# Kernel optimization log

Measured on AMD Instinct MI355X. Metric: run time of the kernel, lower is better.

Reference implementation:

```python
import jax, jax.numpy as jnp
import numpy as np

ALPHA = 20.0  # SuperSpike surrogate sharpness
V_TH = 1.0
DT = 1.0

@jax.custom_vjp
def heaviside(x):
    return (x > 0).astype(x.dtype)

def _heaviside_fwd(x):
    return heaviside(x), x

def _heaviside_bwd(x, g):
    # SuperSpike surrogate gradient: 1 / (alpha*|x| + 1)^2
    return (g / (ALPHA * jnp.abs(x) + 1.0) ** 2,)

heaviside.defvjp(_heaviside_fwd, _heaviside_bwd)


def setup_inputs() -> dict:
    key = jax.random.key(0)
    k1, k2 = jax.random.split(key)
    B, T, IN, H = 128, 2000, 16, 256
    x = jax.random.normal(k1, (B, T, IN), dtype=jnp.float32)
    W = jax.random.normal(k2, (H, IN), dtype=jnp.float32) / np.sqrt(IN)
    tau_syn = jnp.full((1, H), 0.1, dtype=jnp.float32)
    tau_mem = jnp.full((1, H), 0.05, dtype=jnp.float32)
    return {"x": x, "W": W, "tau_syn": tau_syn, "tau_mem": tau_mem}


def reference(x, W, tau_syn, tau_mem):
    """SNNEncode forward: linear input projection + LIF recurrence over time.
    x: [B,T,IN], W: [H,IN], taus: [1,H]. Returns (spikes [T,B,H], (v,i) final state)."""
    tau_syn_inv = jnp.clip(tau_syn, 0.0, 1.0)  # [1,H]
    tau_mem_inv = jnp.clip(tau_mem, 0.0, 1.0)  # [1,H]

    B, T, IN = x.shape
    H = W.shape[0]
    # project all timesteps at once: [T,B,H]
    xw = jnp.einsum("bti,hi->tbh", x, W)

    def step(state, inp_t):
        v, i = state
        # norse lif_feed_forward_step (v_leak = 0, v_reset = 0)
        v_dec = v + DT * tau_mem_inv * (-v + i)
        i_dec = i + DT * (-tau_syn_inv) * i
        z = heaviside(v_dec - V_TH)
        v_new = (1.0 - z) * v_dec
        i_new = i_dec + inp_t
        return (v_new, i_new), z

    zeros = jnp.zeros((B, H), dtype=x.dtype)
    (v_f, i_f), spikes = jax.lax.scan(step, (zeros, zeros), xw)
    return spikes, v_f, i_f
```

## Files before the change

kernel.cpp:

```cpp
#include <hip/hip_runtime.h>


constexpr int B  = 128;
constexpr int T  = 2000;
constexpr int IN = 16;
constexpr int H  = 256;
constexpr int BH = B * H;
constexpr int CH = 256;

typedef float f4 __attribute__((ext_vector_type(4)));

__global__ __launch_bounds__(128, 1) void snn_named(
    const float* __restrict__ x, const float* __restrict__ Wm,
    const float* __restrict__ tau_syn, const float* __restrict__ tau_mem,
    float* __restrict__ out)
{
#pragma clang fp contract(off)
  const int tid = threadIdx.x, bid = blockIdx.x;
  const int b = bid >> 1;
  const int h = ((bid & 1) << 7) | tid;

  float w[IN];
#pragma unroll
  for (int k = 0; k < IN; ++k) w[k] = Wm[h * IN + k];

  float ts = tau_syn[h]; ts = ts < 0.f ? 0.f : (ts > 1.f ? 1.f : ts);
  float tm = tau_mem[h]; tm = tm < 0.f ? 0.f : (tm > 1.f ? 1.f : tm);
  const float nts = -ts;

  const char* xbc = (const char*)(x + (size_t)b * T * IN);
  const f4*   xb4 = (const f4*)xbc;
  float* op = out + (size_t)b * H + h;
  float vS = 0.f, iS = 0.f;

  auto TOUCH = [&](int r0) {
    const int lim = T * 4 - 1;
#pragma unroll
    for (int i = 0; i < 8; ++i) {
      int idx = r0 * 4 + tid + i * 128;
      idx = idx > lim ? lim : idx;
      f4 d = xb4[idx];
      asm volatile("" :: "v"(d.x), "v"(d.y), "v"(d.z), "v"(d.w));
    }
  };

  f4 A0, A1, A2, A3, A4, A5, A6, A7;
  f4 Bg0, Bg1, Bg2, Bg3, Bg4, Bg5, Bg6, Bg7;
  f4 C0, C1, C2, C3, C4, C5, C6, C7;
  f4 D0, D1, D2, D3, D4, D5, D6, D7;

#define LOADG(P0_, P1_, P2_, P3_, P4_, P5_, P6_, P7_, r)                 \
  do {                                                                   \
    int ra_ = (r);                                                       \
    ra_ = ra_ > (T - 2) ? (T - 2) : ra_;                                 \
    int off_ = ra_ * (IN * 4);                                           \
    asm("" : "+v"(off_));                  \
    const f4* q_ = (const f4*)(xbc + off_);                              \
    P0_ = q_[0]; P1_ = q_[1]; P2_ = q_[2]; P3_ = q_[3];                  \
    P4_ = q_[4]; P5_ = q_[5]; P6_ = q_[6]; P7_ = q_[7];                  \
  } while (0)

#define LIF1(xwv)                                                        \
  do {                                                                   \
    const float t1_ = iS - vS;                                           \
    const float t2_ = tm * t1_;                                          \
    const float vd_ = vS + t2_;                                          \
    const float xm_ = vd_ - 1.0f;                                        \
    const bool  sp_ = xm_ > 0.0f;                                        \
    vS = sp_ ? 0.0f : vd_;                                               \
    const float t3_ = nts * iS;                                          \
    const float id_ = iS + t3_;                                          \
    iS = id_ + (xwv);                                                    \
    __builtin_nontemporal_store(sp_ ? 1.0f : 0.0f, op);                  \
    op += BH;                                                            \
  } while (0)

#define DOT4(Q0_, Q1_, Q2_, Q3_, dst_)                                   \
  do {                                                                   \
    float a_ = 0.0f;                                                     \
    a_ = __builtin_fmaf(Q0_[0], w[0],  a_);                              \
    a_ = __builtin_fmaf(Q0_[1], w[1],  a_);                              \
    a_ = __builtin_fmaf(Q0_[2], w[2],  a_);                              \
    a_ = __builtin_fmaf(Q0_[3], w[3],  a_);                              \
    a_ = __builtin_fmaf(Q1_[0], w[4],  a_);                              \
    a_ = __builtin_fmaf(Q1_[1], w[5],  a_);                              \
    a_ = __builtin_fmaf(Q1_[2], w[6],  a_);                              \
    a_ = __builtin_fmaf(Q1_[3], w[7],  a_);                              \
    a_ = __builtin_fmaf(Q2_[0], w[8],  a_);                              \
    a_ = __builtin_fmaf(Q2_[1], w[9],  a_);                              \
    a_ = __builtin_fmaf(Q2_[2], w[10], a_);                              \
    a_ = __builtin_fmaf(Q2_[3], w[11], a_);                              \
    a_ = __builtin_fmaf(Q3_[0], w[12], a_);                              \
    a_ = __builtin_fmaf(Q3_[1], w[13], a_);                              \
    a_ = __builtin_fmaf(Q3_[2], w[14], a_);                              \
    a_ = __builtin_fmaf(Q3_[3], w[15], a_);                              \
    dst_ = a_;                                                           \
  } while (0)

#define STEP2G(P0_, P1_, P2_, P3_, P4_, P5_, P6_, P7_)                   \
  do {                                                                   \
    float xwa_, xwb_;                                                    \
    DOT4(P0_, P1_, P2_, P3_, xwa_);                                      \
    DOT4(P4_, P5_, P6_, P7_, xwb_);                                      \
    LIF1(xwa_);                                                          \
    LIF1(xwb_);                                                          \
  } while (0)

  TOUCH(0);
  TOUCH(CH);
  LOADG(A0, A1, A2, A3, A4, A5, A6, A7, 0);
  LOADG(Bg0, Bg1, Bg2, Bg3, Bg4, Bg5, Bg6, Bg7, 2);
  LOADG(C0, C1, C2, C3, C4, C5, C6, C7, 4);
  LOADG(D0, D1, D2, D3, D4, D5, D6, D7, 6);

  for (int t0 = 0; t0 < T; t0 += 8) {
    if ((t0 & (CH - 1)) == 0) TOUCH(t0 + 2 * CH);
    STEP2G(A0, A1, A2, A3, A4, A5, A6, A7);
    LOADG(A0, A1, A2, A3, A4, A5, A6, A7, t0 + 8);
    STEP2G(Bg0, Bg1, Bg2, Bg3, Bg4, Bg5, Bg6, Bg7);
    LOADG(Bg0, Bg1, Bg2, Bg3, Bg4, Bg5, Bg6, Bg7, t0 + 10);
    STEP2G(C0, C1, C2, C3, C4, C5, C6, C7);
    LOADG(C0, C1, C2, C3, C4, C5, C6, C7, t0 + 12);
    STEP2G(D0, D1, D2, D3, D4, D5, D6, D7);
    LOADG(D0, D1, D2, D3, D4, D5, D6, D7, t0 + 14);
  }

  out[(size_t)T * BH + (size_t)b * H + h]      = vS;
  out[(size_t)T * BH + BH + (size_t)b * H + h] = iS;
}

extern "C" void kernel_launch(void* const* d_in, const int* in_sizes, int n_in,
                              void* d_out, int out_size, void* d_ws, size_t ws_size,
                              hipStream_t stream) {
  const float* x  = (const float*)d_in[0];
  const float* W  = (const float*)d_in[1];
  const float* ts = (const float*)d_in[2];
  const float* tm = (const float*)d_in[3];
  float* out = (float*)d_out;
  hipLaunchKernelGGL(snn_named, dim3(B * 2), dim3(128), 0, stream,
                     x, W, ts, tm, out);
}
```

Baseline: 447.4 us.

## Buffer spike bits in a register and store them one tile late

Spike flags are no longer stored on every step. Each one is packed into a 32-bit register, and the previous tile's 32 spikes are written out interleaved with the next tile's compute, which takes store issue off the serial recurrence. The L2 prefetch is also reworked from an 8-load touch every 256 steps to a single-load touch per 32-step tile. In exchange the code gains tail handling for the last 16 steps and more complex index math, with some risk of off-by-one errors in the delayed stores.

```diff
diff --git a/kernel.cpp b/kernel.cpp
--- a/kernel.cpp
+++ b/kernel.cpp
@@ -6,11 +6,13 @@
 constexpr int IN = 16;
 constexpr int H  = 256;
 constexpr int BH = B * H;
-constexpr int CH = 256;
+constexpr int TILE = 32;
+constexpr int NTILE = 62;
+constexpr int TAIL = 16;
 
 typedef float f4 __attribute__((ext_vector_type(4)));
 
-__global__ __launch_bounds__(128, 1) void snn_named(
+__global__ __launch_bounds__(128, 1) void snn_bl(
     const float* __restrict__ x, const float* __restrict__ Wm,
     const float* __restrict__ tau_syn, const float* __restrict__ tau_mem,
     float* __restrict__ out)
@@ -30,10 +32,11 @@
 
   const char* xbc = (const char*)(x + (size_t)b * T * IN);
   const f4*   xb4 = (const f4*)xbc;
-  float* op = out + (size_t)b * H + h;
+  float* ob = out + (size_t)b * H + h;
   float vS = 0.f, iS = 0.f;
-
-  auto TOUCH = [&](int r0) {
+  unsigned bits = 0u, bitsPrev = 0u;
+
+  auto TOUCH8 = [&](int r0) {
     const int lim = T * 4 - 1;
 #pragma unroll
     for (int i = 0; i < 8; ++i) {
@@ -43,6 +46,13 @@
       asm volatile("" :: "v"(d.x), "v"(d.y), "v"(d.z), "v"(d.w));
     }
   };
+  auto TOUCH1 = [&](int r0) {
+    const int lim = T * 4 - 1;
+    int idx = r0 * 4 + tid;
+    idx = idx > lim ? lim : idx;
+    f4 d = xb4[idx];
+    asm volatile("" :: "v"(d.x), "v"(d.y), "v"(d.z), "v"(d.w));
+  };
 
   f4 A0, A1, A2, A3, A4, A5, A6, A7;
   f4 Bg0, Bg1, Bg2, Bg3, Bg4, Bg5, Bg6, Bg7;
@@ -54,7 +64,7 @@
     int ra_ = (r);                                                       \
     ra_ = ra_ > (T - 2) ? (T - 2) : ra_;                                 \
     int off_ = ra_ * (IN * 4);                                           \
-    asm("" : "+v"(off_));                  \
+    asm("" : "+v"(off_));                 \
     const f4* q_ = (const f4*)(xbc + off_);                              \
     P0_ = q_[0]; P1_ = q_[1]; P2_ = q_[2]; P3_ = q_[3];                  \
     P4_ = q_[4]; P5_ = q_[5]; P6_ = q_[6]; P7_ = q_[7];                  \
@@ -71,8 +81,7 @@
     const float t3_ = nts * iS;                                          \
     const float id_ = iS + t3_;                                          \
     iS = id_ + (xwv);                                                    \
-    __builtin_nontemporal_store(sp_ ? 1.0f : 0.0f, op);                  \
-    op += BH;                                                            \
+    bits = (bits >> 1) | (sp_ ? 0x80000000u : 0u);                       \
   } while (0)
 
 #define DOT4(Q0_, Q1_, Q2_, Q3_, dst_)                                   \
@@ -106,15 +115,56 @@
     LIF1(xwb_);                                                          \
   } while (0)
 
-  TOUCH(0);
-  TOUCH(CH);
+#define STORE8(t0_, r_)                                                  \
+  do {                                                                   \
+    _Pragma("unroll")                                                    \
+    for (int j_ = 0; j_ < 8; ++j_) {                                     \
+      int rr_ = (t0_) - TILE + 8 * (r_) + j_;                            \
+      rr_ = rr_ < 0 ? 0 : rr_;                                           \
+      const float fv_ =                                                  \
+          ((bitsPrev >> (8 * (r_) + j_)) & 1u) ? 1.0f : 0.0f;            \
+      __builtin_nontemporal_store(fv_, ob + ((size_t)rr_ << 15));        \
+    }                                                                    \
+  } while (0)
+
+  TOUCH8(0);
+  TOUCH8(256);
   LOADG(A0, A1, A2, A3, A4, A5, A6, A7, 0);
   LOADG(Bg0, Bg1, Bg2, Bg3, Bg4, Bg5, Bg6, Bg7, 2);
   LOADG(C0, C1, C2, C3, C4, C5, C6, C7, 4);
   LOADG(D0, D1, D2, D3, D4, D5, D6, D7, 6);
 
-  for (int t0 = 0; t0 < T; t0 += 8) {
-    if ((t0 & (CH - 1)) == 0) TOUCH(t0 + 2 * CH);
+#define ROT(t0_, r_)                                                     \
+  do {                                                                   \
+    STORE8(t0_, r_);                                                     \
+    STEP2G(A0, A1, A2, A3, A4, A5, A6, A7);                              \
+    LOADG(A0, A1, A2, A3, A4, A5, A6, A7, (t0_) + 8 * (r_) + 8);         \
+    STEP2G(Bg0, Bg1, Bg2, Bg3, Bg4, Bg5, Bg6, Bg7);                      \
+    LOADG(Bg0, Bg1, Bg2, Bg3, Bg4, Bg5, Bg6, Bg7, (t0_) + 8 * (r_) + 10);\
+    STEP2G(C0, C1, C2, C3, C4, C5, C6, C7);                              \
+    LOADG(C0, C1, C2, C3, C4, C5, C6, C7, (t0_) + 8 * (r_) + 12);        \
+    STEP2G(D0, D1, D2, D3, D4, D5, D6, D7);                              \
+    LOADG(D0, D1, D2, D3, D4, D5, D6, D7, (t0_) + 8 * (r_) + 14);        \
+  } while (0)
+
+  for (int tile = 0; tile < NTILE; ++tile) {
+    const int t0 = tile * TILE;
+    TOUCH1(t0 + 512);
+    ROT(t0, 0);
+    ROT(t0, 1);
+    ROT(t0, 2);
+    ROT(t0, 3);
+    bitsPrev = bits;
+  }
+
+  {
+    const int t0 = NTILE * TILE;
+#pragma unroll
+    for (int j = 0; j < 32; ++j) {
+      const int rr = t0 - TILE + j;
+      const float fv = ((bitsPrev >> j) & 1u) ? 1.0f : 0.0f;
+      __builtin_nontemporal_store(fv, ob + ((size_t)rr << 15));
+    }
     STEP2G(A0, A1, A2, A3, A4, A5, A6, A7);
     LOADG(A0, A1, A2, A3, A4, A5, A6, A7, t0 + 8);
     STEP2G(Bg0, Bg1, Bg2, Bg3, Bg4, Bg5, Bg6, Bg7);
@@ -123,6 +173,16 @@
     LOADG(C0, C1, C2, C3, C4, C5, C6, C7, t0 + 12);
     STEP2G(D0, D1, D2, D3, D4, D5, D6, D7);
     LOADG(D0, D1, D2, D3, D4, D5, D6, D7, t0 + 14);
+    STEP2G(A0, A1, A2, A3, A4, A5, A6, A7);
+    STEP2G(Bg0, Bg1, Bg2, Bg3, Bg4, Bg5, Bg6, Bg7);
+    STEP2G(C0, C1, C2, C3, C4, C5, C6, C7);
+    STEP2G(D0, D1, D2, D3, D4, D5, D6, D7);
+#pragma unroll
+    for (int j = 0; j < 16; ++j) {
+      const int rr = t0 + j;
+      const float fv = ((bits >> (16 + j)) & 1u) ? 1.0f : 0.0f;
+      __builtin_nontemporal_store(fv, ob + ((size_t)rr << 15));
+    }
   }
 
   out[(size_t)T * BH + (size_t)b * H + h]      = vS;
@@ -137,6 +197,6 @@
   const float* ts = (const float*)d_in[2];
   const float* tm = (const float*)d_in[3];
   float* out = (float*)d_out;
-  hipLaunchKernelGGL(snn_named, dim3(B * 2), dim3(128), 0, stream,
+  hipLaunchKernelGGL(snn_bl, dim3(B * 2), dim3(128), 0, stream,
                      x, W, ts, tm, out);
 }
```

Result: slower. 460.0 us (+2.8%).
